# Performance work log

Hardware: AMD Instinct MI355X
Metric: run time of the kernel (lower is better)

## Reference

```python
import jax, jax.numpy as jnp
import numpy as np

B, T, CIN, H, W = 8, 16, 16, 64, 64
HID, K = 64, 3


def _conv(x, w, b):
    # x: [B, C, H, W], w: [O, C, K, K] -> [B, O, H, W], 'same' padding
    y = jax.lax.conv_general_dilated(x, w, window_strides=(1, 1), padding='SAME',
                                     dimension_numbers=('NCHW', 'OIHW', 'NCHW'))
    return y + b[None, :, None, None]


def setup_inputs() -> dict:
    key = jax.random.key(0)
    ks = jax.random.split(key, 9)
    cin_h = CIN + HID
    s_conv = 1.0 / np.sqrt(cin_h * K * K)
    s_lin = 1.0 / np.sqrt(cin_h)
    return {
        'x': jax.random.normal(ks[0], (B, T, CIN, H, W), dtype=jnp.float32),
        'Wf': jax.random.uniform(ks[1], (HID, cin_h, K, K), jnp.float32, -s_conv, s_conv),
        'bf': jax.random.uniform(ks[2], (HID,), jnp.float32, -s_conv, s_conv),
        'Wi': jax.random.uniform(ks[3], (HID, cin_h, K, K), jnp.float32, -s_conv, s_conv),
        'bi': jax.random.uniform(ks[4], (HID,), jnp.float32, -s_conv, s_conv),
        'Wc': jax.random.uniform(ks[5], (HID, cin_h, K, K), jnp.float32, -s_conv, s_conv),
        'bc': jax.random.uniform(ks[6], (HID,), jnp.float32, -s_conv, s_conv),
        'Wo': jax.random.uniform(ks[7], (HID, cin_h), jnp.float32, -s_lin, s_lin),
        'bo': jax.random.uniform(ks[8], (HID,), jnp.float32, -s_lin, s_lin),
    }


def reference(x, Wf, bf, Wi, bi, Wc, bc, Wo, bo):
    # x: [B, T, CIN, H, W]
    b, t, cin, h, w = x.shape
    h0 = jnp.zeros((b, HID, h, w), x.dtype)
    c0 = jnp.zeros((b, HID, h, w), x.dtype)

    def step(carry, xt):
        hs, cs = carry
        xc = jnp.concatenate([xt, hs], axis=1)          # [B, CIN+HID, H, W]
        f = jax.nn.sigmoid(_conv(xc, Wf, bf))
        i = jax.nn.sigmoid(_conv(xc, Wi, bi))
        g = jnp.tanh(_conv(xc, Wc, bc))
        # Linear over channel dim (torch applies it on transpose(1,3))
        o = jax.nn.sigmoid(jnp.einsum('bchw,oc->bohw', xc, Wo) + bo[None, :, None, None])
        cs = cs * f + i * g
        hs = jnp.tanh(cs) * o
        return (hs, cs), None

    xs = jnp.swapaxes(x, 0, 1)                          # time-major [T, B, CIN, H, W]
    (hT, cT), _ = jax.lax.scan(step, (h0, c0), xs)
    return hT, cT
```

## Files before the change

kernel.cpp:

```cpp
#include <hip/hip_runtime.h>


#define B_ 8
#define T_ 16
#define CIN_ 16
#define HID_ 64
#define H_ 64
#define W_ 64
#define HW_ (H_*W_)
#define CTOT_ 80
#define XS_ROW 66
#define XS_CH 104
#define XS_SIZE (4*XS_ROW*XS_CH)
#define CSTRIDE_ (B_*HID_*HW_)

typedef __attribute__((ext_vector_type(8))) short short8;
typedef __attribute__((ext_vector_type(4))) float f32x4;

__device__ __forceinline__ unsigned short f2bf(float f){
    unsigned u = __float_as_uint(f);
    u = (u + 0x7FFFu + ((u >> 16) & 1u)) >> 16;
    return (unsigned short)u;
}
__device__ __forceinline__ float sigm_(float v){ return 1.0f/(1.0f + __expf(-v)); }
__device__ __forceinline__ float tanh_(float v){ return 2.0f/(1.0f + __expf(-2.0f*v)) - 1.0f; }

__global__ void prep_wfrag(const float* __restrict__ Wf, const float* __restrict__ Wi,
                           const float* __restrict__ Wc, const float* __restrict__ Wo,
                           const float* __restrict__ bf, const float* __restrict__ bi,
                           const float* __restrict__ bc, const float* __restrict__ bo,
                           unsigned short* __restrict__ Wfrag){
    int idx = blockIdx.x*256 + threadIdx.x;
    int j    = idx & 7;
    int lane = (idx >> 3) & 63;
    int frag = idx >> 9;
    int ng = frag & 15;
    int tc = frag >> 4;
    int cc = tc % 3, tap = tc / 3;
    int n = ng*16 + (lane & 15);
    int g = n >> 6, o = n & 63;
    int c = cc*32 + ((lane >> 4) << 3) + j;
    int ky = tap / 3, kx = tap % 3;
    float v = 0.0f;
    if (c < CTOT_){
        if (g == 0)      v = Wf[((o*CTOT_ + c)*3 + ky)*3 + kx];
        else if (g == 1) v = Wi[((o*CTOT_ + c)*3 + ky)*3 + kx];
        else if (g == 2) v = Wc[((o*CTOT_ + c)*3 + ky)*3 + kx];
        else             v = (tap == 4) ? Wo[o*CTOT_ + c] : 0.0f;
    } else if (c == CTOT_ && tap == 4){
        v = (g==0) ? bf[o] : (g==1) ? bi[o] : (g==2) ? bc[o] : bo[o];
    }
    Wfrag[idx] = f2bf(v);
}

__global__ void prep_xbf(const float* __restrict__ x, unsigned short* __restrict__ xbf){
    int idx = blockIdx.x*256 + threadIdx.x;
    int px = idx & 63;
    int y  = (idx >> 6) & 63;
    int bt = idx >> 12;
    const float* src = x + (size_t)bt*CIN_*HW_ + y*W_ + px;
    unsigned short tmp[16];
    #pragma unroll
    for (int c = 0; c < 16; ++c) tmp[c] = f2bf(src[(size_t)c*HW_]);
    uint4* dst = (uint4*)(xbf + (size_t)idx*16);
    dst[0] = *(uint4*)(tmp);
    dst[1] = *(uint4*)(tmp + 8);
}

__global__ __launch_bounds__(512, 2) void lstm_step(
    const unsigned short* __restrict__ xbf,
    const unsigned short* __restrict__ Wfrag,
    float* __restrict__ cbuf,
    const unsigned short* __restrict__ hin,
    unsigned short* __restrict__ hout,
    float* __restrict__ out,
    int t)
{
    __shared__ __align__(16) unsigned short Xs[XS_SIZE];
    const int id   = blockIdx.x;
    const int xcd  = id & 7;
    const int j    = id >> 3;
    const int b    = j >> 2;
    const int y0   = xcd*8 + ((j & 3) << 1);
    const int tid  = threadIdx.x;
    const int lane = tid & 63;
    const int wid  = tid >> 6;
    const int wm   = wid >> 2;
    const int wn   = wid & 3;
    const int l15  = lane & 15;
    const int q    = lane >> 4;

    uint4 z4; z4.x=z4.y=z4.z=z4.w=0u;
    for (int i = tid; i < XS_SIZE/8; i += 512) ((uint4*)Xs)[i] = z4;
    __syncthreads();

    {
        int row = tid >> 7, rem = tid & 127;
        int px = rem >> 1, ch8 = rem & 1;
        int yy = y0 + row - 1;
        if (yy >= 0 && yy < H_){
            uint4 v = *(const uint4*)(xbf + ((((size_t)(b*T_ + t)*H_ + yy)*W_ + px)*16 + ch8*8));
            *(uint4*)(Xs + ((size_t)(row*XS_ROW + px + 1))*XS_CH + ch8*8) = v;
        }
    }
    if (t > 0){
        #pragma unroll
        for (int k = 0; k < 4; ++k){
            int i = tid + (k << 9);
            int row = i >> 9, rem = i & 511;
            int px = rem >> 3, ch8 = rem & 7;
            int yy = y0 + row - 1;
            if (yy >= 0 && yy < H_){
                uint4 v = *(const uint4*)(hin + ((((size_t)b*H_ + yy)*W_ + px)*HID_ + ch8*8));
                *(uint4*)(Xs + (size_t)(row*XS_ROW + px + 1)*XS_CH + CIN_ + ch8*8) = v;
            }
        }
    }
    for (int i = tid; i < 4*XS_ROW; i += 512)
        Xs[i*XS_CH + CTOT_] = 0x3F80;
    __syncthreads();

    f32x4 acc[4][4];
    #pragma unroll
    for (int g = 0; g < 4; ++g){
        #pragma unroll
        for (int mf = 0; mf < 4; ++mf) acc[g][mf] = (f32x4)0.0f;
    }

    const unsigned short* Abase = Xs + (size_t)(wm*XS_ROW + l15)*XS_CH + q*8;
    const unsigned short* Bbase = Wfrag + (size_t)wn*512 + lane*8;

    short8 a[3][4], bb[3][3], bO[3];
    #pragma unroll
    for (int p = 0; p < 2; ++p){
        const int tap = p/3, cc = p%3;
        const int ky = tap/3, kx = tap%3;
        const int aoff = (ky*XS_ROW + kx)*XS_CH + cc*32;
        #pragma unroll
        for (int mf = 0; mf < 4; ++mf)
            a[p][mf] = *(const short8*)(Abase + aoff + mf*16*XS_CH);
        #pragma unroll
        for (int g = 0; g < 3; ++g)
            bb[p][g] = *(const short8*)(Bbase + p*8192 + g*2048);
    }

    #pragma unroll
    for (int tc = 0; tc < 27; ++tc){
        const int tap = tc/3;
        const int cur = tc % 3;
        if (tc + 2 < 27){
            const int ntc = tc + 2;
            const int nxt = ntc % 3;
            const int ntap = ntc/3, ncc = ntc%3;
            const int nky = ntap/3, nkx = ntap%3;
            const int aoff = (nky*XS_ROW + nkx)*XS_CH + ncc*32;
            #pragma unroll
            for (int mf = 0; mf < 4; ++mf)
                a[nxt][mf] = *(const short8*)(Abase + aoff + mf*16*XS_CH);
            #pragma unroll
            for (int g = 0; g < 3; ++g)
                bb[nxt][g] = *(const short8*)(Bbase + ntc*8192 + g*2048);
        }
        if (tc >= 10 && tc <= 12)
            bO[tc-10] = *(const short8*)(Bbase + (tc+2)*8192 + 6144);
        if (tap == 4){
            #pragma unroll
            for (int mf = 0; mf < 4; ++mf)
                acc[3][mf] = __builtin_amdgcn_mfma_f32_16x16x32_bf16(a[cur][mf], bO[tc-12], acc[3][mf], 0,0,0);
        }
        #pragma unroll
        for (int g = 0; g < 3; ++g){
            #pragma unroll
            for (int mf = 0; mf < 4; ++mf)
                acc[g][mf] = __builtin_amdgcn_mfma_f32_16x16x32_bf16(a[cur][mf], bb[cur][g], acc[g][mf], 0,0,0);
        }
    }

    const int o = wn*16 + l15;
    const int y = y0 + wm;
    #pragma unroll
    for (int mf = 0; mf < 4; ++mf){
        #pragma unroll
        for (int r = 0; r < 4; ++r){
            const int px = mf*16 + q*4 + r;
            const float fv = sigm_(acc[0][mf][r]);
            const float iv = sigm_(acc[1][mf][r]);
            const float gv = tanh_(acc[2][mf][r]);
            const float ov = sigm_(acc[3][mf][r]);
            const size_t cidx = (((size_t)(b*H_ + y)*W_ + px)*HID_ + o);
            const float cprev = t ? cbuf[cidx] : 0.0f;
            const float cn = cprev*fv + iv*gv;
            const float hn = tanh_(cn)*ov;
            if (t < T_-1){
                cbuf[cidx] = cn;
                hout[cidx] = f2bf(hn);
            } else {
                const size_t oidx = ((((size_t)(b*HID_ + o))*H_ + y)*W_ + px);
                out[oidx] = hn;
                out[CSTRIDE_ + oidx] = cn;
            }
        }
    }
}

extern "C" void kernel_launch(void* const* d_in, const int* in_sizes, int n_in,
                              void* d_out, int out_size, void* d_ws, size_t ws_size,
                              hipStream_t stream){
    const float* x  = (const float*)d_in[0];
    const float* Wf = (const float*)d_in[1];
    const float* bf = (const float*)d_in[2];
    const float* Wi = (const float*)d_in[3];
    const float* bi = (const float*)d_in[4];
    const float* Wc = (const float*)d_in[5];
    const float* bc = (const float*)d_in[6];
    const float* Wo = (const float*)d_in[7];
    const float* bo = (const float*)d_in[8];

    unsigned short* Wfrag = (unsigned short*)d_ws;
    unsigned short* xbf   = (unsigned short*)((char*)d_ws + 442368);
    float*          cbuf  = (float*)((char*)d_ws + 442368 + 16777216);
    unsigned short* hbfA  = (unsigned short*)((char*)d_ws + 442368 + 16777216 + 8388608);
    unsigned short* hbfB  = hbfA + CSTRIDE_;

    prep_wfrag<<<dim3(864), dim3(256), 0, stream>>>(Wf, Wi, Wc, Wo, bf, bi, bc, bo, Wfrag);
    prep_xbf<<<dim3(2048), dim3(256), 0, stream>>>(x, xbf);

    for (int t = 0; t < T_; ++t){
        const unsigned short* hi = (t & 1) ? hbfA : hbfB;
        unsigned short*       ho = (t & 1) ? hbfB : hbfA;
        lstm_step<<<dim3(256), dim3(512), 0, stream>>>(
            xbf, Wfrag, cbuf, hi, ho, (float*)d_out, t);
    }
}
```

Baseline: 396.9 us.

## Fuse timestep launches into persistent kernel with neighbor flag synchronization

Replaces the sixteen per-timestep launches with one persistent kernel of 256 blocks. Blocks loop over time and sync only with their up and down row neighbours through global atomic flags, and the cell state stays in registers instead of a global buffer. This removes launch overhead, the global barrier between steps, and the c-state global traffic. In exchange it depends on all 256 blocks being co-resident (launch bounds drop to one block per CU), and spin-waits can stall or deadlock if they are not.

```diff
diff --git a/kernel.cpp b/kernel.cpp
--- a/kernel.cpp
+++ b/kernel.cpp
@@ -25,11 +25,23 @@
 __device__ __forceinline__ float sigm_(float v){ return 1.0f/(1.0f + __expf(-v)); }
 __device__ __forceinline__ float tanh_(float v){ return 2.0f/(1.0f + __expf(-2.0f*v)) - 1.0f; }
 
+__device__ __forceinline__ void wait_ge(int* f, int v){
+    while (__hip_atomic_load(f, __ATOMIC_RELAXED, __HIP_MEMORY_SCOPE_AGENT) < v)
+        __builtin_amdgcn_s_sleep(2);
+}
+__device__ __forceinline__ void st_flag(int* f, int v){
+    __hip_atomic_store(f, v, __ATOMIC_RELEASE, __HIP_MEMORY_SCOPE_AGENT);
+}
+
 __global__ void prep_wfrag(const float* __restrict__ Wf, const float* __restrict__ Wi,
                            const float* __restrict__ Wc, const float* __restrict__ Wo,
                            const float* __restrict__ bf, const float* __restrict__ bi,
                            const float* __restrict__ bc, const float* __restrict__ bo,
-                           unsigned short* __restrict__ Wfrag){
+                           unsigned short* __restrict__ Wfrag, int* __restrict__ flags){
+    if (blockIdx.x == 0){
+        flags[threadIdx.x]       = 0;
+        flags[256 + threadIdx.x] = 0;
+    }
     int idx = blockIdx.x*256 + threadIdx.x;
     int j    = idx & 7;
     int lane = (idx >> 3) & 63;
@@ -67,21 +79,26 @@
     dst[1] = *(uint4*)(tmp + 8);
 }
 
-__global__ __launch_bounds__(512, 2) void lstm_step(
+__global__ __launch_bounds__(512, 1) void lstm_persist(
     const unsigned short* __restrict__ xbf,
     const unsigned short* __restrict__ Wfrag,
-    float* __restrict__ cbuf,
-    const unsigned short* __restrict__ hin,
-    unsigned short* __restrict__ hout,
+    unsigned short* __restrict__ hbA,
+    unsigned short* __restrict__ hbB,
     float* __restrict__ out,
-    int t)
+    int* __restrict__ flags)
 {
     __shared__ __align__(16) unsigned short Xs[XS_SIZE];
+    int* fdone = flags;
+    int* fstag = flags + 256;
+
     const int id   = blockIdx.x;
     const int xcd  = id & 7;
     const int j    = id >> 3;
     const int b    = j >> 2;
     const int y0   = xcd*8 + ((j & 3) << 1);
+    const int yp   = xcd*4 + (j & 3);
+    const int bu   = (yp > 0)  ? (((b*4 + ((yp-1)&3)) << 3) | ((yp-1) >> 2)) : -1;
+    const int bd   = (yp < 31) ? (((b*4 + ((yp+1)&3)) << 3) | ((yp+1) >> 2)) : -1;
     const int tid  = threadIdx.x;
     const int lane = tid & 63;
     const int wid  = tid >> 6;
@@ -92,113 +109,148 @@
 
     uint4 z4; z4.x=z4.y=z4.z=z4.w=0u;
     for (int i = tid; i < XS_SIZE/8; i += 512) ((uint4*)Xs)[i] = z4;
-    __syncthreads();
-
-    {
-        int row = tid >> 7, rem = tid & 127;
-        int px = rem >> 1, ch8 = rem & 1;
-        int yy = y0 + row - 1;
-        if (yy >= 0 && yy < H_){
-            uint4 v = *(const uint4*)(xbf + ((((size_t)(b*T_ + t)*H_ + yy)*W_ + px)*16 + ch8*8));
-            *(uint4*)(Xs + ((size_t)(row*XS_ROW + px + 1))*XS_CH + ch8*8) = v;
-        }
-    }
-    if (t > 0){
-        #pragma unroll
-        for (int k = 0; k < 4; ++k){
-            int i = tid + (k << 9);
-            int row = i >> 9, rem = i & 511;
-            int px = rem >> 3, ch8 = rem & 7;
+
+    float cr[4][4];
+    #pragma unroll
+    for (int mf = 0; mf < 4; ++mf)
+        #pragma unroll
+        for (int r = 0; r < 4; ++r) cr[mf][r] = 0.0f;
+
+    const unsigned short* Abase = Xs + (size_t)(wm*XS_ROW + l15)*XS_CH + q*8;
+    const unsigned short* Bbase = Wfrag + (size_t)wn*512 + lane*8;
+    const int o = wn*16 + l15;
+    const int y = y0 + wm;
+
+    #pragma unroll 1
+    for (int t = 0; t < T_; ++t){
+        const unsigned short* hi = (t & 1) ? hbA : hbB;
+        unsigned short*       ho = (t & 1) ? hbB : hbA;
+
+        if (t > 0 && tid == 0){
+            if (bu >= 0) wait_ge(fdone + bu, t);
+            if (bd >= 0) wait_ge(fdone + bd, t);
+            __threadfence();
+        }
+        __syncthreads();
+
+        if (t == 0){
+            for (int i = tid; i < 4*XS_ROW; i += 512)
+                Xs[i*XS_CH + CTOT_] = 0x3F80;
+        }
+        uint4 hv[4]; bool hok[4] = {false,false,false,false};
+        int hrow[4], hpx[4], hch8[4];
+        if (t > 0){
+            #pragma unroll
+            for (int k = 0; k < 4; ++k){
+                int i = tid + (k << 9);
+                hrow[k] = i >> 9; int rem = i & 511; hpx[k] = rem >> 3; hch8[k] = rem & 7;
+                int yy = y0 + hrow[k] - 1;
+                if (yy >= 0 && yy < H_){
+                    hok[k] = true;
+                    hv[k] = *(const uint4*)(hi + ((((size_t)b*H_ + yy)*W_ + hpx[k])*HID_ + hch8[k]*8));
+                }
+            }
+        }
+        {
+            int row = tid >> 7, rem = tid & 127;
+            int px = rem >> 1, ch8 = rem & 1;
             int yy = y0 + row - 1;
             if (yy >= 0 && yy < H_){
-                uint4 v = *(const uint4*)(hin + ((((size_t)b*H_ + yy)*W_ + px)*HID_ + ch8*8));
-                *(uint4*)(Xs + (size_t)(row*XS_ROW + px + 1)*XS_CH + CIN_ + ch8*8) = v;
-            }
-        }
-    }
-    for (int i = tid; i < 4*XS_ROW; i += 512)
-        Xs[i*XS_CH + CTOT_] = 0x3F80;
-    __syncthreads();
-
-    f32x4 acc[4][4];
-    #pragma unroll
-    for (int g = 0; g < 4; ++g){
-        #pragma unroll
-        for (int mf = 0; mf < 4; ++mf) acc[g][mf] = (f32x4)0.0f;
-    }
-
-    const unsigned short* Abase = Xs + (size_t)(wm*XS_ROW + l15)*XS_CH + q*8;
-    const unsigned short* Bbase = Wfrag + (size_t)wn*512 + lane*8;
-
-    short8 a[3][4], bb[3][3], bO[3];
-    #pragma unroll
-    for (int p = 0; p < 2; ++p){
-        const int tap = p/3, cc = p%3;
-        const int ky = tap/3, kx = tap%3;
-        const int aoff = (ky*XS_ROW + kx)*XS_CH + cc*32;
-        #pragma unroll
-        for (int mf = 0; mf < 4; ++mf)
-            a[p][mf] = *(const short8*)(Abase + aoff + mf*16*XS_CH);
-        #pragma unroll
-        for (int g = 0; g < 3; ++g)
-            bb[p][g] = *(const short8*)(Bbase + p*8192 + g*2048);
-    }
-
-    #pragma unroll
-    for (int tc = 0; tc < 27; ++tc){
-        const int tap = tc/3;
-        const int cur = tc % 3;
-        if (tc + 2 < 27){
-            const int ntc = tc + 2;
-            const int nxt = ntc % 3;
-            const int ntap = ntc/3, ncc = ntc%3;
-            const int nky = ntap/3, nkx = ntap%3;
-            const int aoff = (nky*XS_ROW + nkx)*XS_CH + ncc*32;
+                uint4 v = *(const uint4*)(xbf + ((((size_t)(b*T_ + t)*H_ + yy)*W_ + px)*16 + ch8*8));
+                *(uint4*)(Xs + ((size_t)(row*XS_ROW + px + 1))*XS_CH + ch8*8) = v;
+            }
+        }
+        if (t > 0){
+            #pragma unroll
+            for (int k = 0; k < 4; ++k)
+                if (hok[k])
+                    *(uint4*)(Xs + (size_t)(hrow[k]*XS_ROW + hpx[k] + 1)*XS_CH + CIN_ + hch8[k]*8) = hv[k];
+        }
+        __syncthreads();
+        if (t > 0 && tid == 0) st_flag(fstag + id, t + 1);
+
+        f32x4 acc[4][4];
+        #pragma unroll
+        for (int g = 0; g < 4; ++g){
+            #pragma unroll
+            for (int mf = 0; mf < 4; ++mf) acc[g][mf] = (f32x4)0.0f;
+        }
+        short8 a[3][4], bb[3][3], bO[3];
+        #pragma unroll
+        for (int p = 0; p < 2; ++p){
+            const int tap = p/3, cc = p%3;
+            const int ky = tap/3, kx = tap%3;
+            const int aoff = (ky*XS_ROW + kx)*XS_CH + cc*32;
             #pragma unroll
             for (int mf = 0; mf < 4; ++mf)
-                a[nxt][mf] = *(const short8*)(Abase + aoff + mf*16*XS_CH);
+                a[p][mf] = *(const short8*)(Abase + aoff + mf*16*XS_CH);
             #pragma unroll
             for (int g = 0; g < 3; ++g)
-                bb[nxt][g] = *(const short8*)(Bbase + ntc*8192 + g*2048);
-        }
-        if (tc >= 10 && tc <= 12)
-            bO[tc-10] = *(const short8*)(Bbase + (tc+2)*8192 + 6144);
-        if (tap == 4){
-            #pragma unroll
-            for (int mf = 0; mf < 4; ++mf)
-                acc[3][mf] = __builtin_amdgcn_mfma_f32_16x16x32_bf16(a[cur][mf], bO[tc-12], acc[3][mf], 0,0,0);
-        }
-        #pragma unroll
-        for (int g = 0; g < 3; ++g){
-            #pragma unroll
-            for (int mf = 0; mf < 4; ++mf)
-                acc[g][mf] = __builtin_amdgcn_mfma_f32_16x16x32_bf16(a[cur][mf], bb[cur][g], acc[g][mf], 0,0,0);
-        }
-    }
-
-    const int o = wn*16 + l15;
-    const int y = y0 + wm;
-    #pragma unroll
-    for (int mf = 0; mf < 4; ++mf){
-        #pragma unroll
-        for (int r = 0; r < 4; ++r){
-            const int px = mf*16 + q*4 + r;
-            const float fv = sigm_(acc[0][mf][r]);
-            const float iv = sigm_(acc[1][mf][r]);
-            const float gv = tanh_(acc[2][mf][r]);
-            const float ov = sigm_(acc[3][mf][r]);
-            const size_t cidx = (((size_t)(b*H_ + y)*W_ + px)*HID_ + o);
-            const float cprev = t ? cbuf[cidx] : 0.0f;
-            const float cn = cprev*fv + iv*gv;
-            const float hn = tanh_(cn)*ov;
-            if (t < T_-1){
-                cbuf[cidx] = cn;
-                hout[cidx] = f2bf(hn);
-            } else {
-                const size_t oidx = ((((size_t)(b*HID_ + o))*H_ + y)*W_ + px);
-                out[oidx] = hn;
-                out[CSTRIDE_ + oidx] = cn;
-            }
+                bb[p][g] = *(const short8*)(Bbase + p*8192 + g*2048);
+        }
+        #pragma unroll
+        for (int tc = 0; tc < 27; ++tc){
+            const int tap = tc/3;
+            const int cur = tc % 3;
+            if (tc + 2 < 27){
+                const int ntc = tc + 2;
+                const int nxt = ntc % 3;
+                const int ntap = ntc/3, ncc = ntc%3;
+                const int nky = ntap/3, nkx = ntap%3;
+                const int aoff = (nky*XS_ROW + nkx)*XS_CH + ncc*32;
+                #pragma unroll
+                for (int mf = 0; mf < 4; ++mf)
+                    a[nxt][mf] = *(const short8*)(Abase + aoff + mf*16*XS_CH);
+                #pragma unroll
+                for (int g = 0; g < 3; ++g)
+                    bb[nxt][g] = *(const short8*)(Bbase + ntc*8192 + g*2048);
+            }
+            if (tc >= 10 && tc <= 12)
+                bO[tc-10] = *(const short8*)(Bbase + (tc+2)*8192 + 6144);
+            if (tap == 4){
+                #pragma unroll
+                for (int mf = 0; mf < 4; ++mf)
+                    acc[3][mf] = __builtin_amdgcn_mfma_f32_16x16x32_bf16(a[cur][mf], bO[tc-12], acc[3][mf], 0,0,0);
+            }
+            #pragma unroll
+            for (int g = 0; g < 3; ++g){
+                #pragma unroll
+                for (int mf = 0; mf < 4; ++mf)
+                    acc[g][mf] = __builtin_amdgcn_mfma_f32_16x16x32_bf16(a[cur][mf], bb[cur][g], acc[g][mf], 0,0,0);
+            }
+        }
+
+        if (t >= 2 && tid == 0){
+            if (bu >= 0) wait_ge(fstag + bu, t);
+            if (bd >= 0) wait_ge(fstag + bd, t);
+        }
+        __syncthreads();
+
+        #pragma unroll
+        for (int mf = 0; mf < 4; ++mf){
+            #pragma unroll
+            for (int r = 0; r < 4; ++r){
+                const int px = mf*16 + q*4 + r;
+                const float fv = sigm_(acc[0][mf][r]);
+                const float iv = sigm_(acc[1][mf][r]);
+                const float gv = tanh_(acc[2][mf][r]);
+                const float ov = sigm_(acc[3][mf][r]);
+                const float cn = cr[mf][r]*fv + iv*gv;
+                const float hn = tanh_(cn)*ov;
+                cr[mf][r] = cn;
+                if (t < T_-1){
+                    ho[(((size_t)(b*H_ + y)*W_ + px)*HID_ + o)] = f2bf(hn);
+                } else {
+                    const size_t oidx = ((((size_t)(b*HID_ + o))*H_ + y)*W_ + px);
+                    out[oidx] = hn;
+                    out[CSTRIDE_ + oidx] = cn;
+                }
+            }
+        }
+        __syncthreads();
+        if (t < T_-1 && tid == 0){
+            __threadfence();
+            st_flag(fdone + id, t + 1);
         }
     }
 }
@@ -218,17 +270,11 @@
 
     unsigned short* Wfrag = (unsigned short*)d_ws;
     unsigned short* xbf   = (unsigned short*)((char*)d_ws + 442368);
-    float*          cbuf  = (float*)((char*)d_ws + 442368 + 16777216);
-    unsigned short* hbfA  = (unsigned short*)((char*)d_ws + 442368 + 16777216 + 8388608);
-    unsigned short* hbfB  = hbfA + CSTRIDE_;
-
-    prep_wfrag<<<dim3(864), dim3(256), 0, stream>>>(Wf, Wi, Wc, Wo, bf, bi, bc, bo, Wfrag);
+    unsigned short* hbA   = (unsigned short*)((char*)d_ws + 17219584);
+    unsigned short* hbB   = (unsigned short*)((char*)d_ws + 21413888);
+    int*            flags = (int*)((char*)d_ws + 25608192);
+
+    prep_wfrag<<<dim3(864), dim3(256), 0, stream>>>(Wf, Wi, Wc, Wo, bf, bi, bc, bo, Wfrag, flags);
     prep_xbf<<<dim3(2048), dim3(256), 0, stream>>>(x, xbf);
-
-    for (int t = 0; t < T_; ++t){
-        const unsigned short* hi = (t & 1) ? hbfA : hbfB;
-        unsigned short*       ho = (t & 1) ? hbfB : hbfA;
-        lstm_step<<<dim3(256), dim3(512), 0, stream>>>(
-            xbf, Wfrag, cbuf, hi, ho, (float*)d_out, t);
-    }
-}
+    lstm_persist<<<dim3(256), dim3(512), 0, stream>>>(xbf, Wfrag, hbA, hbB, (float*)d_out, flags);
+}
```

Result: slower. 1.134 ms (+185.8%).
